# Kernel tuning notes

Measured on AMD Instinct MI355X. Metric: run time of the kernel, lower is better.

The kernel has to match this reference:

```python
import jax, jax.numpy as jnp
import numpy as np

MARGIN = 1.0
EPS = 1e-16


def setup_inputs() -> dict:
    key = jax.random.key(0)
    k1, k2 = jax.random.split(key)
    B, E = 512, 128
    embs = jax.random.normal(k1, (B, E), dtype=jnp.float32)
    labels = jax.random.randint(k2, (B,), 0, 64, dtype=jnp.int64)
    return {"embs": embs, "labels": labels}


def _triplet_mask(labels):
    # [B,B,B] mask: valid (a,p,n) iff a!=p, a!=n, p!=n, label[a]==label[p], label[a]!=label[n]
    B = labels.shape[0]
    neq = ~jnp.eye(B, dtype=bool)
    idx_mask = neq[:, :, None] & neq[:, None, :] & neq[None, :, :]
    lab_eq = labels[:, None] == labels[None, :]
    lab_mask = lab_eq[:, :, None] & (~lab_eq)[:, None, :]
    return idx_mask & lab_mask


def reference(embs, labels):
    # pairwise squared L2 distances (squared=True path, no sqrt)
    dot = embs @ embs.T                      # [B,B]
    sq_norm = jnp.diagonal(dot)              # [B]
    dist = sq_norm[:, None] - 2.0 * dot + sq_norm[None, :]
    dist = jnp.maximum(dist, 0.0)            # [B,B]

    # triplet losses: d(a,p) - d(a,n) + margin, over [B,B,B]
    triplet_loss = dist[:, :, None] - dist[:, None, :] + MARGIN
    mask = _triplet_mask(labels)
    triplet_loss = jnp.maximum(triplet_loss * mask.astype(triplet_loss.dtype), 0.0)

    n_pos = jnp.sum(triplet_loss > EPS)
    return jnp.sum(triplet_loss) / (n_pos.astype(triplet_loss.dtype) + EPS)
```

## Files before the change

### kernel.cpp

```cpp
#include <hip/hip_runtime.h>


#define BSZ 512
#define EDIM 128
#define TS 32
#define NPOSMAX 96

__global__ __launch_bounds__(256) void dist_tiles(
    const float* __restrict__ embs,
    float* __restrict__ D)
{
    __shared__ float At[TS][EDIM + 4];
    __shared__ float Bt[TS][EDIM + 4];
    __shared__ float nA[TS], nB[TS];

    const int tid = threadIdx.x;
    const int bi = blockIdx.x >> 4;
    const int bj = blockIdx.x & 15;
    const int I = bi * TS, J = bj * TS;

#pragma unroll
    for (int q = 0; q < 4; ++q) {
        int idx = tid + 256 * q;
        int r   = idx >> 5;
        int k4  = idx & 31;
        float4 va = reinterpret_cast<const float4*>(embs + (size_t)(I + r) * EDIM)[k4];
        *reinterpret_cast<float4*>(&At[r][k4 * 4]) = va;
        float4 vb = reinterpret_cast<const float4*>(embs + (size_t)(J + r) * EDIM)[k4];
        *reinterpret_cast<float4*>(&Bt[r][k4 * 4]) = vb;
    }
    __syncthreads();

    if (tid < 64) {
        int r = tid & 31;
        float s = 0.f;
        if (tid < 32) {
#pragma unroll
            for (int k = 0; k < EDIM; k += 4) {
                float4 v = *reinterpret_cast<float4*>(&At[r][k]);
                s += v.x * v.x + v.y * v.y + v.z * v.z + v.w * v.w;
            }
            nA[r] = s;
        } else {
#pragma unroll
            for (int k = 0; k < EDIM; k += 4) {
                float4 v = *reinterpret_cast<float4*>(&Bt[r][k]);
                s += v.x * v.x + v.y * v.y + v.z * v.z + v.w * v.w;
            }
            nB[r] = s;
        }
    }
    __syncthreads();

    const int tr = tid >> 4, tc = tid & 15;
    float a00 = 0.f, a01 = 0.f, a10 = 0.f, a11 = 0.f;
#pragma unroll 8
    for (int k = 0; k < EDIM; k += 4) {
        float4 x0 = *reinterpret_cast<float4*>(&At[tr][k]);
        float4 x1 = *reinterpret_cast<float4*>(&At[tr + 16][k]);
        float4 y0 = *reinterpret_cast<float4*>(&Bt[tc][k]);
        float4 y1 = *reinterpret_cast<float4*>(&Bt[tc + 16][k]);
        a00 += x0.x * y0.x + x0.y * y0.y + x0.z * y0.z + x0.w * y0.w;
        a01 += x0.x * y1.x + x0.y * y1.y + x0.z * y1.z + x0.w * y1.w;
        a10 += x1.x * y0.x + x1.y * y0.y + x1.z * y0.z + x1.w * y0.w;
        a11 += x1.x * y1.x + x1.y * y1.y + x1.z * y1.z + x1.w * y1.w;
    }
    float* Drow0 = D + (size_t)(I + tr) * BSZ + J;
    float* Drow1 = D + (size_t)(I + tr + 16) * BSZ + J;
    Drow0[tc]      = fmaxf(nA[tr]      + nB[tc]      - 2.f * a00, 0.f);
    Drow0[tc + 16] = fmaxf(nA[tr]      + nB[tc + 16] - 2.f * a01, 0.f);
    Drow1[tc]      = fmaxf(nA[tr + 16] + nB[tc]      - 2.f * a10, 0.f);
    Drow1[tc + 16] = fmaxf(nA[tr + 16] + nB[tc + 16] - 2.f * a11, 0.f);
}

__global__ __launch_bounds__(256) void triplet_pass(
    const float* __restrict__ D,
    const int* __restrict__ labels,
    float* __restrict__ sums,
    float* __restrict__ cnts)
{
    __shared__ int   lab[BSZ];
    __shared__ float d[BSZ];
    __shared__ unsigned long long masks[8];
    __shared__ int   plist[NPOSMAX];
    __shared__ float wsum[4];
    __shared__ int   wcnt[4];

    const int a = blockIdx.x, tid = threadIdx.x;
    const int wv = tid >> 6, lane = tid & 63;

    lab[tid]       = labels[tid];
    lab[tid + 256] = labels[tid + 256];
    float2 dv = reinterpret_cast<const float2*>(D + (size_t)a * BSZ)[tid];
    d[tid * 2]     = dv.x;
    d[tid * 2 + 1] = dv.y;
    __syncthreads();

    const int la = lab[a];

#pragma unroll
    for (int c = 0; c < 2; ++c) {
        int j = c * 256 + tid;
        unsigned long long m = __ballot(lab[j] == la && j != a);
        if (lane == 0) masks[c * 4 + wv] = m;
    }
    __syncthreads();

    int np = 0;
#pragma unroll
    for (int m = 0; m < 8; ++m) np += __popcll(masks[m]);
    if (np > NPOSMAX) np = NPOSMAX;

#pragma unroll
    for (int c = 0; c < 2; ++c) {
        int j = c * 256 + tid;
        if (lab[j] == la && j != a) {
            int mi = c * 4 + wv, off = 0;
            for (int m = 0; m < mi; ++m) off += __popcll(masks[m]);
            off += __popcll(masks[mi] & ((1ull << lane) - 1ull));
            if (off < NPOSMAX) plist[off] = j;
        }
    }
    __syncthreads();

    float s = 0.f;
    int   cnt = 0;
#pragma unroll
    for (int c = 0; c < 2; ++c) {
        int n = c * 256 + tid;
        if (lab[n] != la) {
            float dn = d[n];
            for (int i = 0; i < np; ++i) {
                float t = fmaxf(d[plist[i]] - dn + 1.0f, 0.f);
                s += t;
                cnt += (t > 1e-16f) ? 1 : 0;
            }
        }
    }

#pragma unroll
    for (int off = 32; off; off >>= 1) {
        s   += __shfl_down(s, off);
        cnt += __shfl_down(cnt, off);
    }
    if (lane == 0) { wsum[wv] = s; wcnt[wv] = cnt; }
    __syncthreads();
    if (tid == 0) {
        sums[a] = wsum[0] + wsum[1] + wsum[2] + wsum[3];
        cnts[a] = (float)(wcnt[0] + wcnt[1] + wcnt[2] + wcnt[3]);
    }
}

__global__ __launch_bounds__(512) void finalize(
    const float* __restrict__ sums,
    const float* __restrict__ cnts,
    float* __restrict__ out)
{
    __shared__ float wsum[8], wcnt[8];
    const int tid = threadIdx.x;
    float s = sums[tid];
    float c = cnts[tid];
#pragma unroll
    for (int off = 32; off; off >>= 1) {
        s += __shfl_down(s, off);
        c += __shfl_down(c, off);
    }
    const int wv = tid >> 6, lane = tid & 63;
    if (lane == 0) { wsum[wv] = s; wcnt[wv] = c; }
    __syncthreads();
    if (tid == 0) {
        float S = 0.f, C = 0.f;
#pragma unroll
        for (int w = 0; w < 8; ++w) { S += wsum[w]; C += wcnt[w]; }
        out[0] = S / (C + 1e-16f);
    }
}

extern "C" void kernel_launch(void* const* d_in, const int* in_sizes, int n_in,
                              void* d_out, int out_size, void* d_ws, size_t ws_size,
                              hipStream_t stream)
{
    const float* embs   = reinterpret_cast<const float*>(d_in[0]);
    const int*   labels = reinterpret_cast<const int*>(d_in[1]);
    float*       out    = reinterpret_cast<float*>(d_out);

    float* D    = reinterpret_cast<float*>(d_ws);
    float* sums = D + (size_t)BSZ * BSZ;
    float* cnts = sums + BSZ;

    dist_tiles<<<256, 256, 0, stream>>>(embs, D);
    triplet_pass<<<BSZ, 256, 0, stream>>>(D, labels, sums, cnts);
    finalize<<<1, 512, 0, stream>>>(sums, cnts, out);
}
```

Measured before the change: 16.32 us.

## Precompute positive distances and fuse hinge loss into distance tile kernel

Adds a first kernel that, for each anchor, builds its positive list and computes anchor-positive squared distances directly from the embeddings into a compact per-anchor buffer. The hinge loss is then evaluated inside the GEMM distance tile kernel, where each computed anchor-negative distance is looped against that anchor's stored positive distances. This removes the full 512x512 distance matrix write and re-read and the per-anchor triplet pass. In exchange, the tile kernel loads more shared memory and does per-thread loops whose trip counts vary. NPOSMAX also drops from 96 to 64, which silently truncates anchors with more positives. Positive distances now come from a direct difference rather than the norm-expansion formula, so they can differ slightly in rounding.

```diff
diff --git a/kernel.cpp b/kernel.cpp
--- a/kernel.cpp
+++ b/kernel.cpp
@@ -4,20 +4,87 @@
 #define BSZ 512
 #define EDIM 128
 #define TS 32
-#define NPOSMAX 96
-
-__global__ __launch_bounds__(256) void dist_tiles(
+#define NPOSMAX 64
+
+__global__ __launch_bounds__(256) void pos_dists(
     const float* __restrict__ embs,
-    float* __restrict__ D)
+    const int* __restrict__ labels,
+    float* __restrict__ posd,
+    int* __restrict__ npos)
+{
+    __shared__ int lab[BSZ];
+    __shared__ unsigned long long masks[8];
+    __shared__ int plist[NPOSMAX];
+
+    const int a = blockIdx.x, tid = threadIdx.x;
+    const int wv = tid >> 6, lane = tid & 63;
+
+    lab[tid]       = labels[tid];
+    lab[tid + 256] = labels[tid + 256];
+    __syncthreads();
+
+    const int la = lab[a];
+
+#pragma unroll
+    for (int c = 0; c < 2; ++c) {
+        int j = c * 256 + tid;
+        unsigned long long m = __ballot(lab[j] == la && j != a);
+        if (lane == 0) masks[c * 4 + wv] = m;
+    }
+    __syncthreads();
+
+    int np = 0;
+#pragma unroll
+    for (int m = 0; m < 8; ++m) np += __popcll(masks[m]);
+    if (np > NPOSMAX) np = NPOSMAX;
+
+#pragma unroll
+    for (int c = 0; c < 2; ++c) {
+        int j = c * 256 + tid;
+        if (lab[j] == la && j != a) {
+            int mi = c * 4 + wv, off = 0;
+            for (int m = 0; m < mi; ++m) off += __popcll(masks[m]);
+            off += __popcll(masks[mi] & ((1ull << lane) - 1ull));
+            if (off < NPOSMAX) plist[off] = j;
+        }
+    }
+    if (tid == 0) npos[a] = np;
+    __syncthreads();
+
+    float2 av = reinterpret_cast<const float2*>(embs + (size_t)a * EDIM)[lane];
+    for (int i = wv; i < np; i += 4) {
+        int p = plist[i];
+        float2 pv = reinterpret_cast<const float2*>(embs + (size_t)p * EDIM)[lane];
+        float dx = av.x - pv.x, dy = av.y - pv.y;
+        float t = dx * dx + dy * dy;
+#pragma unroll
+        for (int off = 32; off; off >>= 1) t += __shfl_xor(t, off);
+        if (lane == 0) posd[(size_t)a * NPOSMAX + i] = t;
+    }
+}
+
+__global__ __launch_bounds__(256) void hinge_tiles(
+    const float* __restrict__ embs,
+    const int* __restrict__ labels,
+    const float* __restrict__ posd,
+    const int* __restrict__ npos,
+    float* __restrict__ sums,
+    float* __restrict__ cnts)
 {
     __shared__ float At[TS][EDIM + 4];
     __shared__ float Bt[TS][EDIM + 4];
     __shared__ float nA[TS], nB[TS];
+    __shared__ float psh[TS][NPOSMAX + 1];
+    __shared__ int   npsh[TS];
+    __shared__ int   labI[TS], labJ[TS];
+    __shared__ float wsum[4];
+    __shared__ int   wcnt[4];
 
     const int tid = threadIdx.x;
     const int bi = blockIdx.x >> 4;
     const int bj = blockIdx.x & 15;
     const int I = bi * TS, J = bj * TS;
+    const int wv = tid >> 6, lane = tid & 63;
 
 #pragma unroll
     for (int q = 0; q < 4; ++q) {
@@ -29,6 +96,14 @@
         float4 vb = reinterpret_cast<const float4*>(embs + (size_t)(J + r) * EDIM)[k4];
         *reinterpret_cast<float4*>(&Bt[r][k4 * 4]) = vb;
     }
+#pragma unroll
+    for (int q = 0; q < 8; ++q) {
+        int idx = tid + 256 * q;
+        int r = idx >> 6, p = idx & 63;
+        psh[r][p] = posd[(size_t)(I + r) * NPOSMAX + p];
+    }
+    if (tid < TS) { npsh[tid] = npos[I + tid]; labI[tid] = labels[I + tid]; }
+    else if (tid < 2 * TS) { labJ[tid - TS] = labels[J + tid - TS]; }
     __syncthreads();
 
     if (tid < 64) {
@@ -65,98 +140,61 @@
         a10 += x1.x * y0.x + x1.y * y0.y + x1.z * y0.z + x1.w * y0.w;
         a11 += x1.x * y1.x + x1.y * y1.y + x1.z * y1.z + x1.w * y1.w;
     }
-    float* Drow0 = D + (size_t)(I + tr) * BSZ + J;
-    float* Drow1 = D + (size_t)(I + tr + 16) * BSZ + J;
-    Drow0[tc]      = fmaxf(nA[tr]      + nB[tc]      - 2.f * a00, 0.f);
-    Drow0[tc + 16] = fmaxf(nA[tr]      + nB[tc + 16] - 2.f * a01, 0.f);
-    Drow1[tc]      = fmaxf(nA[tr + 16] + nB[tc]      - 2.f * a10, 0.f);
-    Drow1[tc + 16] = fmaxf(nA[tr + 16] + nB[tc + 16] - 2.f * a11, 0.f);
-}
-
-__global__ __launch_bounds__(256) void triplet_pass(
-    const float* __restrict__ D,
-    const int* __restrict__ labels,
-    float* __restrict__ sums,
-    float* __restrict__ cnts)
-{
-    __shared__ int   lab[BSZ];
-    __shared__ float d[BSZ];
-    __shared__ unsigned long long masks[8];
-    __shared__ int   plist[NPOSMAX];
-    __shared__ float wsum[4];
-    __shared__ int   wcnt[4];
-
-    const int a = blockIdx.x, tid = threadIdx.x;
-    const int wv = tid >> 6, lane = tid & 63;
-
-    lab[tid]       = labels[tid];
-    lab[tid + 256] = labels[tid + 256];
-    float2 dv = reinterpret_cast<const float2*>(D + (size_t)a * BSZ)[tid];
-    d[tid * 2]     = dv.x;
-    d[tid * 2 + 1] = dv.y;
-    __syncthreads();
-
-    const int la = lab[a];
-
-#pragma unroll
-    for (int c = 0; c < 2; ++c) {
-        int j = c * 256 + tid;
-        unsigned long long m = __ballot(lab[j] == la && j != a);
-        if (lane == 0) masks[c * 4 + wv] = m;
-    }
-    __syncthreads();
-
-    int np = 0;
-#pragma unroll
-    for (int m = 0; m < 8; ++m) np += __popcll(masks[m]);
-    if (np > NPOSMAX) np = NPOSMAX;
-
-#pragma unroll
-    for (int c = 0; c < 2; ++c) {
-        int j = c * 256 + tid;
-        if (lab[j] == la && j != a) {
-            int mi = c * 4 + wv, off = 0;
-            for (int m = 0; m < mi; ++m) off += __popcll(masks[m]);
-            off += __popcll(masks[mi] & ((1ull << lane) - 1ull));
-            if (off < NPOSMAX) plist[off] = j;
-        }
-    }
-    __syncthreads();
+    float d00 = fmaxf(nA[tr]      + nB[tc]      - 2.f * a00, 0.f);
+    float d01 = fmaxf(nA[tr]      + nB[tc + 16] - 2.f * a01, 0.f);
+    float d10 = fmaxf(nA[tr + 16] + nB[tc]      - 2.f * a10, 0.f);
+    float d11 = fmaxf(nA[tr + 16] + nB[tc + 16] - 2.f * a11, 0.f);
+
+    const int la0 = labI[tr], la1 = labI[tr + 16];
+    const int ln0 = labJ[tc], ln1 = labJ[tc + 16];
+    const int np0 = npsh[tr], np1 = npsh[tr + 16];
 
     float s = 0.f;
-    int   cnt = 0;
-#pragma unroll
-    for (int c = 0; c < 2; ++c) {
-        int n = c * 256 + tid;
-        if (lab[n] != la) {
-            float dn = d[n];
-            for (int i = 0; i < np; ++i) {
-                float t = fmaxf(d[plist[i]] - dn + 1.0f, 0.f);
-                s += t;
-                cnt += (t > 1e-16f) ? 1 : 0;
-            }
+    int   c = 0;
+    if (ln0 != la0) {
+        for (int p = 0; p < np0; ++p) {
+            float t = fmaxf(psh[tr][p] - d00 + 1.0f, 0.f);
+            s += t; c += (t > 1e-16f) ? 1 : 0;
+        }
+    }
+    if (ln1 != la0) {
+        for (int p = 0; p < np0; ++p) {
+            float t = fmaxf(psh[tr][p] - d01 + 1.0f, 0.f);
+            s += t; c += (t > 1e-16f) ? 1 : 0;
+        }
+    }
+    if (ln0 != la1) {
+        for (int p = 0; p < np1; ++p) {
+            float t = fmaxf(psh[tr + 16][p] - d10 + 1.0f, 0.f);
+            s += t; c += (t > 1e-16f) ? 1 : 0;
+        }
+    }
+    if (ln1 != la1) {
+        for (int p = 0; p < np1; ++p) {
+            float t = fmaxf(psh[tr + 16][p] - d11 + 1.0f, 0.f);
+            s += t; c += (t > 1e-16f) ? 1 : 0;
         }
     }
 
 #pragma unroll
     for (int off = 32; off; off >>= 1) {
-        s   += __shfl_down(s, off);
-        cnt += __shfl_down(cnt, off);
-    }
-    if (lane == 0) { wsum[wv] = s; wcnt[wv] = cnt; }
+        s += __shfl_down(s, off);
+        c += __shfl_down(c, off);
+    }
+    if (lane == 0) { wsum[wv] = s; wcnt[wv] = c; }
     __syncthreads();
     if (tid == 0) {
-        sums[a] = wsum[0] + wsum[1] + wsum[2] + wsum[3];
-        cnts[a] = (float)(wcnt[0] + wcnt[1] + wcnt[2] + wcnt[3]);
-    }
-}
-
-__global__ __launch_bounds__(512) void finalize(
+        sums[blockIdx.x] = wsum[0] + wsum[1] + wsum[2] + wsum[3];
+        cnts[blockIdx.x] = (float)(wcnt[0] + wcnt[1] + wcnt[2] + wcnt[3]);
+    }
+}
+
+__global__ __launch_bounds__(256) void finalize(
     const float* __restrict__ sums,
     const float* __restrict__ cnts,
     float* __restrict__ out)
 {
-    __shared__ float wsum[8], wcnt[8];
+    __shared__ float wsum[4], wcnt[4];
     const int tid = threadIdx.x;
     float s = sums[tid];
     float c = cnts[tid];
@@ -169,9 +207,8 @@
     if (lane == 0) { wsum[wv] = s; wcnt[wv] = c; }
     __syncthreads();
     if (tid == 0) {
-        float S = 0.f, C = 0.f;
-#pragma unroll
-        for (int w = 0; w < 8; ++w) { S += wsum[w]; C += wcnt[w]; }
+        float S = wsum[0] + wsum[1] + wsum[2] + wsum[3];
+        float C = wcnt[0] + wcnt[1] + wcnt[2] + wcnt[3];
         out[0] = S / (C + 1e-16f);
     }
 }
@@ -184,11 +221,12 @@
     const int*   labels = reinterpret_cast<const int*>(d_in[1]);
     float*       out    = reinterpret_cast<float*>(d_out);
 
-    float* D    = reinterpret_cast<float*>(d_ws);
-    float* sums = D + (size_t)BSZ * BSZ;
-    float* cnts = sums + BSZ;
-
-    dist_tiles<<<256, 256, 0, stream>>>(embs, D);
-    triplet_pass<<<BSZ, 256, 0, stream>>>(D, labels, sums, cnts);
-    finalize<<<1, 512, 0, stream>>>(sums, cnts, out);
-}
+    float* posd  = reinterpret_cast<float*>(d_ws);
+    int*   npos  = reinterpret_cast<int*>(posd + (size_t)BSZ * NPOSMAX);
+    float* sums  = reinterpret_cast<float*>(npos + BSZ);
+    float* cnts  = sums + 256;
+
+    pos_dists<<<BSZ, 256, 0, stream>>>(embs, labels, posd, npos);
+    hinge_tiles<<<256, 256, 0, stream>>>(embs, labels, posd, npos, sums, cnts);
+    finalize<<<1, 256, 0, stream>>>(sums, cnts, out);
+}
```

After: 19.19 us. 1.18x slower.

## Compute pairwise distance tiles with bf16 MFMA and fused norms

Applied to the files above, without the earlier changes.

Replaces the scalar fp32 dot-product loop in the distance kernel with bf16 MFMA 16x16x32 instructions. Embeddings are converted to bf16 as they are staged into shared memory, with -2 folded into the B operand. The squared norms are computed during the load using wave shuffles and used to seed the accumulator. This cuts FMA work and a sync phase, but bf16 rounding of the dot products can flip hinge decisions near the margin and change the loss.

```diff
diff --git a/kernel.cpp b/kernel.cpp
--- a/kernel.cpp
+++ b/kernel.cpp
@@ -1,4 +1,5 @@
 #include <hip/hip_runtime.h>
+#include <hip/hip_bf16.h>
 
 
 #define BSZ 512
@@ -6,71 +7,78 @@
 #define TS 32
 #define NPOSMAX 96
 
-__global__ __launch_bounds__(256) void dist_tiles(
+typedef __attribute__((ext_vector_type(8))) short short8;
+typedef __attribute__((ext_vector_type(4))) float f32x4;
+
+__device__ __forceinline__ unsigned short f2bf(float f) {
+    __hip_bfloat16 h = __float2bfloat16(f);
+    return *reinterpret_cast<unsigned short*>(&h);
+}
+
+__global__ __launch_bounds__(256) void dist_mfma(
     const float* __restrict__ embs,
     float* __restrict__ D)
 {
-    __shared__ float At[TS][EDIM + 4];
-    __shared__ float Bt[TS][EDIM + 4];
+    __shared__ unsigned short Abf[TS][136];
+    __shared__ unsigned short Bbf[TS][136];
     __shared__ float nA[TS], nB[TS];
 
     const int tid = threadIdx.x;
     const int bi = blockIdx.x >> 4;
     const int bj = blockIdx.x & 15;
     const int I = bi * TS, J = bj * TS;
+    const int wv = tid >> 6, lane = tid & 63;
+
+    const float4* E4 = reinterpret_cast<const float4*>(embs);
 
 #pragma unroll
     for (int q = 0; q < 4; ++q) {
         int idx = tid + 256 * q;
         int r   = idx >> 5;
         int k4  = idx & 31;
-        float4 va = reinterpret_cast<const float4*>(embs + (size_t)(I + r) * EDIM)[k4];
-        *reinterpret_cast<float4*>(&At[r][k4 * 4]) = va;
-        float4 vb = reinterpret_cast<const float4*>(embs + (size_t)(J + r) * EDIM)[k4];
-        *reinterpret_cast<float4*>(&Bt[r][k4 * 4]) = vb;
-    }
-    __syncthreads();
-
-    if (tid < 64) {
-        int r = tid & 31;
-        float s = 0.f;
-        if (tid < 32) {
-#pragma unroll
-            for (int k = 0; k < EDIM; k += 4) {
-                float4 v = *reinterpret_cast<float4*>(&At[r][k]);
-                s += v.x * v.x + v.y * v.y + v.z * v.z + v.w * v.w;
-            }
-            nA[r] = s;
-        } else {
-#pragma unroll
-            for (int k = 0; k < EDIM; k += 4) {
-                float4 v = *reinterpret_cast<float4*>(&Bt[r][k]);
-                s += v.x * v.x + v.y * v.y + v.z * v.z + v.w * v.w;
-            }
-            nB[r] = s;
-        }
-    }
-    __syncthreads();
-
-    const int tr = tid >> 4, tc = tid & 15;
-    float a00 = 0.f, a01 = 0.f, a10 = 0.f, a11 = 0.f;
-#pragma unroll 8
-    for (int k = 0; k < EDIM; k += 4) {
-        float4 x0 = *reinterpret_cast<float4*>(&At[tr][k]);
-        float4 x1 = *reinterpret_cast<float4*>(&At[tr + 16][k]);
-        float4 y0 = *reinterpret_cast<float4*>(&Bt[tc][k]);
-        float4 y1 = *reinterpret_cast<float4*>(&Bt[tc + 16][k]);
-        a00 += x0.x * y0.x + x0.y * y0.y + x0.z * y0.z + x0.w * y0.w;
-        a01 += x0.x * y1.x + x0.y * y1.y + x0.z * y1.z + x0.w * y1.w;
-        a10 += x1.x * y0.x + x1.y * y0.y + x1.z * y0.z + x1.w * y0.w;
-        a11 += x1.x * y1.x + x1.y * y1.y + x1.z * y1.z + x1.w * y1.w;
-    }
-    float* Drow0 = D + (size_t)(I + tr) * BSZ + J;
-    float* Drow1 = D + (size_t)(I + tr + 16) * BSZ + J;
-    Drow0[tc]      = fmaxf(nA[tr]      + nB[tc]      - 2.f * a00, 0.f);
-    Drow0[tc + 16] = fmaxf(nA[tr]      + nB[tc + 16] - 2.f * a01, 0.f);
-    Drow1[tc]      = fmaxf(nA[tr + 16] + nB[tc]      - 2.f * a10, 0.f);
-    Drow1[tc + 16] = fmaxf(nA[tr + 16] + nB[tc + 16] - 2.f * a11, 0.f);
+
+        float4 va = E4[(size_t)(I + r) * (EDIM / 4) + k4];
+        float sa = va.x * va.x + va.y * va.y + va.z * va.z + va.w * va.w;
+        sa += __shfl_xor(sa, 1); sa += __shfl_xor(sa, 2); sa += __shfl_xor(sa, 4);
+        sa += __shfl_xor(sa, 8); sa += __shfl_xor(sa, 16);
+        if ((tid & 31) == 0) nA[r] = sa;
+        ushort4 ua = { f2bf(va.x), f2bf(va.y), f2bf(va.z), f2bf(va.w) };
+        *reinterpret_cast<ushort4*>(&Abf[r][k4 * 4]) = ua;
+
+        float4 vb = E4[(size_t)(J + r) * (EDIM / 4) + k4];
+        float sb = vb.x * vb.x + vb.y * vb.y + vb.z * vb.z + vb.w * vb.w;
+        sb += __shfl_xor(sb, 1); sb += __shfl_xor(sb, 2); sb += __shfl_xor(sb, 4);
+        sb += __shfl_xor(sb, 8); sb += __shfl_xor(sb, 16);
+        if ((tid & 31) == 0) nB[r] = sb;
+        ushort4 ub = { f2bf(-2.f * vb.x), f2bf(-2.f * vb.y),
+                       f2bf(-2.f * vb.z), f2bf(-2.f * vb.w) };
+        *reinterpret_cast<ushort4*>(&Bbf[r][k4 * 4]) = ub;
+    }
+    __syncthreads();
+
+    const int qi = wv >> 1, qj = wv & 1;
+    const int l15 = lane & 15, lk = lane >> 4;
+
+    f32x4 acc;
+#pragma unroll
+    for (int reg = 0; reg < 4; ++reg)
+        acc[reg] = nA[qi * 16 + lk * 4 + reg] + nB[qj * 16 + l15];
+
+    const unsigned short* arow = &Abf[qi * 16 + l15][0];
+    const unsigned short* brow = &Bbf[qj * 16 + l15][0];
+#pragma unroll
+    for (int ks = 0; ks < 4; ++ks) {
+        short8 af = *reinterpret_cast<const short8*>(arow + ks * 32 + lk * 8);
+        short8 bf = *reinterpret_cast<const short8*>(brow + ks * 32 + lk * 8);
+        acc = __builtin_amdgcn_mfma_f32_16x16x32_bf16(af, bf, acc, 0, 0, 0);
+    }
+
+#pragma unroll
+    for (int reg = 0; reg < 4; ++reg) {
+        int row = I + qi * 16 + lk * 4 + reg;
+        int col = J + qj * 16 + l15;
+        D[(size_t)row * BSZ + col] = fmaxf(acc[reg], 0.f);
+    }
 }
 
 __global__ __launch_bounds__(256) void triplet_pass(
@@ -188,7 +196,7 @@
     float* sums = D + (size_t)BSZ * BSZ;
     float* cnts = sums + BSZ;
 
-    dist_tiles<<<256, 256, 0, stream>>>(embs, D);
+    dist_mfma<<<256, 256, 0, stream>>>(embs, D);
     triplet_pass<<<BSZ, 256, 0, stream>>>(D, labels, sums, cnts);
     finalize<<<1, 512, 0, stream>>>(sums, cnts, out);
 }
```

Result: faster. 15.78 us (-3.4%).
